# Kernel tuning notes

Hardware: AMD Instinct MI355X
Metric: run time of the kernel (lower is better)

The kernel has to match this reference:

```python
import jax, jax.numpy as jnp
import numpy as np
import math

HIDDEN = 1024
HEADS = 16
HEAD_DIM = HIDDEN // HEADS
B, S = 2, 2048


def _xavier(key, shape):
    fan_in, fan_out = shape[1], shape[0]
    limit = math.sqrt(6.0 / (fan_in + fan_out))
    return jax.random.uniform(key, shape, jnp.float32, -limit, limit)


def setup_inputs() -> dict:
    key = jax.random.key(0)
    ks = jax.random.split(key, 5)
    x = jax.random.normal(ks[0], (B, S, HIDDEN), jnp.float32)
    # torch Linear stores weight as [out, in]; y = x @ W.T + b
    Wq = _xavier(ks[1], (HIDDEN, HIDDEN))
    Wk = _xavier(ks[2], (HIDDEN, HIDDEN))
    Wv = _xavier(ks[3], (HIDDEN, HIDDEN))
    Wo = _xavier(ks[4], (HIDDEN, HIDDEN))
    bq = jnp.zeros((HIDDEN,), jnp.float32)
    bk = jnp.zeros((HIDDEN,), jnp.float32)
    bv = jnp.zeros((HIDDEN,), jnp.float32)
    bo = jnp.zeros((HIDDEN,), jnp.float32)
    return {"x": x, "Wq": Wq, "bq": bq, "Wk": Wk, "bk": bk,
            "Wv": Wv, "bv": bv, "Wo": Wo, "bo": bo}


def reference(x, Wq, bq, Wk, bk, Wv, bv, Wo, bo):
    b, s, d = x.shape
    h, hd = HEADS, HEAD_DIM
    q = (x @ Wq.T + bq).reshape(b, s, h, hd).transpose(0, 2, 1, 3)  # [b,h,s,hd]
    k = (x @ Wk.T + bk).reshape(b, s, h, hd).transpose(0, 2, 1, 3)
    v = (x @ Wv.T + bv).reshape(b, s, h, hd).transpose(0, 2, 1, 3)
    scores = jnp.einsum('bhqd,bhkd->bhqk', q, k) / math.sqrt(hd)
    causal = jnp.tril(jnp.ones((s, s), bool))
    scores = jnp.where(causal, scores, -jnp.inf)
    attn = jax.nn.softmax(scores, axis=-1)
    out = jnp.einsum('bhqk,bhkd->bhqd', attn, v)  # [b,h,s,hd]
    out = out.transpose(0, 2, 1, 3).reshape(b, s, d)
    return out @ Wo.T + bo
```

## Files before the change

### kernel.cpp

```cpp
#include <hip/hip_runtime.h>
#include <hip/hip_bf16.h>


typedef __hip_bfloat16 bf16;
typedef __attribute__((ext_vector_type(8))) short short8;
typedef __attribute__((ext_vector_type(4))) short short4v;
typedef __attribute__((ext_vector_type(4))) float f32x4;

#define MFMA16(a, b, c) __builtin_amdgcn_mfma_f32_16x16x32_bf16((a), (b), (c), 0, 0, 0)

__device__ __forceinline__ void load_lds16(const void* g, void* l) {
  __builtin_amdgcn_global_load_lds(
      (const __attribute__((address_space(1))) void*)g,
      (__attribute__((address_space(3))) void*)l, 16, 0, 0);
}

__global__ __launch_bounds__(256) void cvt_kernel(
    const float* __restrict__ x, const float* __restrict__ wq,
    const float* __restrict__ wk, const float* __restrict__ wv,
    const float* __restrict__ wo, bf16* __restrict__ xb, bf16* __restrict__ wqb,
    bf16* __restrict__ wkb, bf16* __restrict__ wvb, bf16* __restrict__ wob) {
  const int seg = blockIdx.y;
  const float* src;
  bf16* dst;
  int n;
  if (seg == 0)      { src = x;  dst = xb;  n = 4194304; }
  else if (seg == 1) { src = wq; dst = wqb; n = 1048576; }
  else if (seg == 2) { src = wk; dst = wkb; n = 1048576; }
  else if (seg == 3) { src = wv; dst = wvb; n = 1048576; }
  else               { src = wo; dst = wob; n = 1048576; }
  const int i = (blockIdx.x * 256 + threadIdx.x) * 4;
  if (i >= n) return;
  const float4 v = *(const float4*)(src + i);
  short4v p;
  ((bf16*)&p)[0] = __float2bfloat16(v.x);
  ((bf16*)&p)[1] = __float2bfloat16(v.y);
  ((bf16*)&p)[2] = __float2bfloat16(v.z);
  ((bf16*)&p)[3] = __float2bfloat16(v.w);
  *(short4v*)(dst + i) = p;
}

template <int BM, typename OutT, bool TRANS>
__device__ __forceinline__ void gemm_body(const bf16* __restrict__ X,
                                          const bf16* __restrict__ W,
                                          const float* __restrict__ bias,
                                          OutT* __restrict__ Y, float scale) {
  constexpr int K = 1024, N = 1024;
  constexpr int MI = BM / 32;
  __shared__ bf16 As[BM * 32];
  __shared__ bf16 Bs[128 * 32];
  const int t = threadIdx.x;
  const int lane = t & 63, w = t >> 6;
  const int quad = lane >> 4, r = lane & 15;
  const int m0 = blockIdx.y * BM, n0 = blockIdx.x * 128;
  const int wm = w >> 1, wn = w & 1;

  f32x4 acc[MI][4] = {};

  for (int k0 = 0; k0 < K; k0 += 32) {
    __syncthreads();
#pragma unroll
    for (int p = 0; p < BM / 64; ++p) {
      const int c = p * 256 + w * 64 + lane;
      const int row = c >> 2;
      const int scb = (c & 3) ^ ((row >> 1) & 3);
      load_lds16(X + (size_t)(m0 + row) * K + k0 + scb * 8, As + c * 8);
    }
#pragma unroll
    for (int p = 0; p < 2; ++p) {
      const int c = p * 256 + w * 64 + lane;
      const int row = c >> 2;
      const int scb = (c & 3) ^ ((row >> 1) & 3);
      load_lds16(W + (size_t)(n0 + row) * K + k0 + scb * 8, Bs + c * 8);
    }
    __syncthreads();
    short8 af[MI], bfr[4];
#pragma unroll
    for (int i = 0; i < MI; ++i) {
      const int ra = wm * (MI * 16) + i * 16 + r;
      af[i] = *(const short8*)(As + ra * 32 + ((quad ^ ((ra >> 1) & 3)) * 8));
    }
#pragma unroll
    for (int j = 0; j < 4; ++j) {
      const int rb = wn * 64 + j * 16 + r;
      bfr[j] = *(const short8*)(Bs + rb * 32 + ((quad ^ ((rb >> 1) & 3)) * 8));
    }
#pragma unroll
    for (int i = 0; i < MI; ++i)
#pragma unroll
      for (int j = 0; j < 4; ++j)
        acc[i][j] = MFMA16(af[i], bfr[j], acc[i][j]);
  }
#pragma unroll
  for (int i = 0; i < MI; ++i) {
    const int m = m0 + wm * (MI * 16) + i * 16 + quad * 4;
#pragma unroll
    for (int j = 0; j < 4; ++j) {
      const int n = n0 + wn * 64 + j * 16 + r;
      const float bv = bias[n];
      if constexpr (TRANS) {
        short4v pk;
#pragma unroll
        for (int g = 0; g < 4; ++g)
          ((bf16*)&pk)[g] = __float2bfloat16((acc[i][j][g] + bv) * scale);
        *(short4v*)((bf16*)Y + (size_t)n * 4096 + m) = pk;
      } else {
#pragma unroll
        for (int g = 0; g < 4; ++g) {
          const float val = (acc[i][j][g] + bv) * scale;
          if constexpr (__is_same(OutT, float))
            Y[(size_t)(m + g) * N + n] = val;
          else
            Y[(size_t)(m + g) * N + n] = __float2bfloat16(val);
        }
      }
    }
  }
}

#define QSCALE 0.18033688f

__global__ __launch_bounds__(256) void qkv_kernel(
    const bf16* __restrict__ x, const bf16* __restrict__ Wq,
    const float* __restrict__ bq, const bf16* __restrict__ Wk,
    const float* __restrict__ bk, const bf16* __restrict__ Wv,
    const float* __restrict__ bv, bf16* Qb, bf16* Kb, bf16* Vtg) {
  if (blockIdx.z == 0)      gemm_body<128, bf16, false>(x, Wq, bq, Qb, QSCALE);
  else if (blockIdx.z == 1) gemm_body<128, bf16, false>(x, Wk, bk, Kb, 1.0f);
  else                      gemm_body<128, bf16, true >(x, Wv, bv, Vtg, 1.0f);
}

__global__ __launch_bounds__(256) void proj_kernel(const bf16* __restrict__ X,
                                                   const bf16* __restrict__ W,
                                                   const float* __restrict__ bias,
                                                   float* __restrict__ Y) {
  gemm_body<64, float, false>(X, W, bias, Y, 1.0f);
}

__global__ __launch_bounds__(256) void attn_kernel(const bf16* __restrict__ Qb,
                                                   const bf16* __restrict__ Kb,
                                                   const bf16* __restrict__ Vtg,
                                                   bf16* __restrict__ Ob) {
  const int pair = blockIdx.x, h = blockIdx.y, b = blockIdx.z;
  const int t = threadIdx.x;
  const int lane = t & 63, w = t >> 6;
  const int quad = lane >> 4, r = lane & 15;

  __shared__ bf16 Ks[64 * 64];
  __shared__ bf16 Vt[64 * 64];
  __shared__ bf16 Pl[4][16 * 64];

#pragma unroll 1
  for (int sel = 0; sel < 2; ++sel) {
    const int j = sel ? (31 - pair) : pair;
    const int q0 = j * 64;
    const int qrow = q0 + w * 16 + r;

    short8 qf[2];
#pragma unroll
    for (int ks = 0; ks < 2; ++ks)
      qf[ks] = *(const short8*)(Qb + (size_t)(b * 2048 + qrow) * 1024 + h * 64 +
                                ks * 32 + quad * 8);

    f32x4 o[4] = {};
    float mrow = -1e30f, lrow = 0.f;

    for (int kt = 0; kt <= j; ++kt) {
      const int k0 = kt * 64;
      __syncthreads();
#pragma unroll
      for (int p = 0; p < 2; ++p) {
        const int c = p * 256 + w * 64 + lane;
        const int row = c >> 3;
        const int scb = (c & 7) ^ (row & 7);
        load_lds16(Kb + (size_t)(b * 2048 + k0 + row) * 1024 + h * 64 + scb * 8,
                   Ks + c * 8);
      }
#pragma unroll
      for (int p = 0; p < 2; ++p) {
        const int c = p * 256 + w * 64 + lane;
        const int row = c >> 3;
        const int scb = (c & 7) ^ (row & 7);
        load_lds16(Vtg + (size_t)(h * 64 + row) * 4096 + b * 2048 + k0 + scb * 8,
                   Vt + c * 8);
      }
      __syncthreads();

      f32x4 st[4] = {};
#pragma unroll
      for (int ks = 0; ks < 2; ++ks) {
        short8 kf[4];
#pragma unroll
        for (int mt = 0; mt < 4; ++mt) {
          const int key = mt * 16 + r;
          kf[mt] = *(const short8*)(Ks + key * 64 +
                                    (((ks * 4 + quad) ^ (key & 7)) * 8));
        }
#pragma unroll
        for (int mt = 0; mt < 4; ++mt) st[mt] = MFMA16(kf[mt], qf[ks], st[mt]);
      }

      if (kt == j) {
#pragma unroll
        for (int mt = 0; mt < 4; ++mt)
#pragma unroll
          for (int g = 0; g < 4; ++g) {
            const int key = k0 + mt * 16 + quad * 4 + g;
            if (key > qrow) st[mt][g] = -1e30f;
          }
      }

      float mx = -1e30f;
#pragma unroll
      for (int mt = 0; mt < 4; ++mt)
#pragma unroll
        for (int g = 0; g < 4; ++g) mx = fmaxf(mx, st[mt][g]);
      mx = fmaxf(mx, __shfl_xor(mx, 16));
      mx = fmaxf(mx, __shfl_xor(mx, 32));
      const float mnew = fmaxf(mrow, mx);
      const float alpha = exp2f(mrow - mnew);
      mrow = mnew;
      float sum = 0.f;
#pragma unroll
      for (int mt = 0; mt < 4; ++mt) {
        bf16 pk[4];
#pragma unroll
        for (int g = 0; g < 4; ++g) {
          const float p = exp2f(st[mt][g] - mnew);
          pk[g] = __float2bfloat16(p);
          sum += __bfloat162float(pk[g]);
        }
        const int key8 = mt * 2 + (quad >> 1);
        const int off = r * 64 + ((key8 ^ (r & 7)) * 8) + (quad & 1) * 4;
        *(short4v*)(&Pl[w][off]) = *(const short4v*)pk;
      }
      sum += __shfl_xor(sum, 16);
      sum += __shfl_xor(sum, 32);
      lrow = lrow * alpha + sum;
#pragma unroll
      for (int mt = 0; mt < 4; ++mt)
#pragma unroll
        for (int g = 0; g < 4; ++g) o[mt][g] *= alpha;

      asm volatile("s_waitcnt lgkmcnt(0)" ::: "memory");

#pragma unroll
      for (int ks = 0; ks < 2; ++ks) {
        short8 vf[4], pf;
#pragma unroll
        for (int mt = 0; mt < 4; ++mt) {
          const int d = mt * 16 + r;
          vf[mt] = *(const short8*)(Vt + d * 64 +
                                    (((ks * 4 + quad) ^ (d & 7)) * 8));
        }
        pf = *(const short8*)(Pl[w] + r * 64 + (((ks * 4 + quad) ^ (r & 7)) * 8));
#pragma unroll
        for (int mt = 0; mt < 4; ++mt) o[mt] = MFMA16(vf[mt], pf, o[mt]);
      }
    }

    const float inv = 1.f / lrow;
#pragma unroll
    for (int mt = 0; mt < 4; ++mt) {
      const int d0 = mt * 16 + quad * 4;
      short4v pk;
#pragma unroll
      for (int g = 0; g < 4; ++g)
        ((bf16*)&pk)[g] = __float2bfloat16(o[mt][g] * inv);
      *(short4v*)(Ob + (size_t)(b * 2048 + qrow) * 1024 + h * 64 + d0) = pk;
    }
  }
}

extern "C" void kernel_launch(void* const* d_in, const int* in_sizes, int n_in,
                              void* d_out, int out_size, void* d_ws, size_t ws_size,
                              hipStream_t stream) {
  const float* x  = (const float*)d_in[0];
  const float* Wq = (const float*)d_in[1];
  const float* bq = (const float*)d_in[2];
  const float* Wk = (const float*)d_in[3];
  const float* bk = (const float*)d_in[4];
  const float* Wv = (const float*)d_in[5];
  const float* bv = (const float*)d_in[6];
  const float* Wo = (const float*)d_in[7];
  const float* bo = (const float*)d_in[8];
  float* out = (float*)d_out;

  bf16* xb  = (bf16*)d_ws;
  bf16* wqb = xb  + (size_t)4096 * 1024;
  bf16* wkb = wqb + (size_t)1024 * 1024;
  bf16* wvb = wkb + (size_t)1024 * 1024;
  bf16* wob = wvb + (size_t)1024 * 1024;
  bf16* Qb  = wob + (size_t)1024 * 1024;
  bf16* Kb  = Qb  + (size_t)4096 * 1024;
  bf16* Vtg = Kb  + (size_t)4096 * 1024;
  bf16* Ob  = Vtg + (size_t)4096 * 1024;
  const size_t need = ((size_t)4096 * 1024 * 5 + (size_t)1024 * 1024 * 4) * 2;
  if (ws_size < need) return;

  cvt_kernel<<<dim3(4096, 5), 256, 0, stream>>>(x, Wq, Wk, Wv, Wo,
                                                xb, wqb, wkb, wvb, wob);
  qkv_kernel<<<dim3(8, 32, 3), 256, 0, stream>>>(xb, wqb, bq, wkb, bk, wvb, bv,
                                                 Qb, Kb, Vtg);
  attn_kernel<<<dim3(16, 16, 2), 256, 0, stream>>>(Qb, Kb, Vtg, Ob);
  proj_kernel<<<dim3(8, 64, 1), 256, 0, stream>>>(Ob, wob, bo, out);
}
```

Baseline: 203.7 us.

## Double-buffer LDS tiles in GEMM and attention loops to prefetch next tile

Both the projection GEMM and the flash-attention kernel now keep two LDS buffers for their staged tiles. The next K-slice (GEMM) or next K/V tile (attention) is issued with global_load_lds right after the barrier, so the loads overlap the MFMA work on the current buffer. This also removes one barrier per iteration. The cost is double the LDS footprint, which may lower occupancy. Correctness relies on the barrier waiting for the outstanding async LDS loads before the buffer is consumed.

```diff
diff --git a/kernel.cpp b/kernel.cpp
--- a/kernel.cpp
+++ b/kernel.cpp
@@ -47,8 +47,8 @@
                                           OutT* __restrict__ Y, float scale) {
   constexpr int K = 1024, N = 1024;
   constexpr int MI = BM / 32;
-  __shared__ bf16 As[BM * 32];
-  __shared__ bf16 Bs[128 * 32];
+  __shared__ bf16 As[2][BM * 32];
+  __shared__ bf16 Bs[2][128 * 32];
   const int t = threadIdx.x;
   const int lane = t & 63, w = t >> 6;
   const int quad = lane >> 4, r = lane & 15;
@@ -57,33 +57,38 @@
 
   f32x4 acc[MI][4] = {};
 
-  for (int k0 = 0; k0 < K; k0 += 32) {
-    __syncthreads();
+  auto stage = [&](int k0, int buf) {
 #pragma unroll
     for (int p = 0; p < BM / 64; ++p) {
       const int c = p * 256 + w * 64 + lane;
       const int row = c >> 2;
       const int scb = (c & 3) ^ ((row >> 1) & 3);
-      load_lds16(X + (size_t)(m0 + row) * K + k0 + scb * 8, As + c * 8);
+      load_lds16(X + (size_t)(m0 + row) * K + k0 + scb * 8, As[buf] + c * 8);
     }
 #pragma unroll
     for (int p = 0; p < 2; ++p) {
       const int c = p * 256 + w * 64 + lane;
       const int row = c >> 2;
       const int scb = (c & 3) ^ ((row >> 1) & 3);
-      load_lds16(W + (size_t)(n0 + row) * K + k0 + scb * 8, Bs + c * 8);
-    }
+      load_lds16(W + (size_t)(n0 + row) * K + k0 + scb * 8, Bs[buf] + c * 8);
+    }
+  };
+
+  stage(0, 0);
+  int cur = 0;
+  for (int k0 = 0; k0 < K; k0 += 32, cur ^= 1) {
     __syncthreads();
+    if (k0 + 32 < K) stage(k0 + 32, cur ^ 1);
     short8 af[MI], bfr[4];
 #pragma unroll
     for (int i = 0; i < MI; ++i) {
       const int ra = wm * (MI * 16) + i * 16 + r;
-      af[i] = *(const short8*)(As + ra * 32 + ((quad ^ ((ra >> 1) & 3)) * 8));
+      af[i] = *(const short8*)(As[cur] + ra * 32 + ((quad ^ ((ra >> 1) & 3)) * 8));
     }
 #pragma unroll
     for (int j = 0; j < 4; ++j) {
       const int rb = wn * 64 + j * 16 + r;
-      bfr[j] = *(const short8*)(Bs + rb * 32 + ((quad ^ ((rb >> 1) & 3)) * 8));
+      bfr[j] = *(const short8*)(Bs[cur] + rb * 32 + ((quad ^ ((rb >> 1) & 3)) * 8));
     }
 #pragma unroll
     for (int i = 0; i < MI; ++i)
@@ -146,9 +151,28 @@
   const int lane = t & 63, w = t >> 6;
   const int quad = lane >> 4, r = lane & 15;
 
-  __shared__ bf16 Ks[64 * 64];
-  __shared__ bf16 Vt[64 * 64];
+  __shared__ bf16 Ks[2][64 * 64];
+  __shared__ bf16 Vt[2][64 * 64];
   __shared__ bf16 Pl[4][16 * 64];
+
+  auto stageKV = [&](int k0, int buf) {
+#pragma unroll
+    for (int p = 0; p < 2; ++p) {
+      const int c = p * 256 + w * 64 + lane;
+      const int row = c >> 3;
+      const int scb = (c & 7) ^ (row & 7);
+      load_lds16(Kb + (size_t)(b * 2048 + k0 + row) * 1024 + h * 64 + scb * 8,
+                 Ks[buf] + c * 8);
+    }
+#pragma unroll
+    for (int p = 0; p < 2; ++p) {
+      const int c = p * 256 + w * 64 + lane;
+      const int row = c >> 3;
+      const int scb = (c & 7) ^ (row & 7);
+      load_lds16(Vtg + (size_t)(h * 64 + row) * 4096 + b * 2048 + k0 + scb * 8,
+                 Vt[buf] + c * 8);
+    }
+  };
 
 #pragma unroll 1
   for (int sel = 0; sel < 2; ++sel) {
@@ -165,26 +189,14 @@
     f32x4 o[4] = {};
     float mrow = -1e30f, lrow = 0.f;
 
-    for (int kt = 0; kt <= j; ++kt) {
+    __syncthreads();
+    stageKV(0, 0);
+    int cur = 0;
+
+    for (int kt = 0; kt <= j; ++kt, cur ^= 1) {
       const int k0 = kt * 64;
       __syncthreads();
-#pragma unroll
-      for (int p = 0; p < 2; ++p) {
-        const int c = p * 256 + w * 64 + lane;
-        const int row = c >> 3;
-        const int scb = (c & 7) ^ (row & 7);
-        load_lds16(Kb + (size_t)(b * 2048 + k0 + row) * 1024 + h * 64 + scb * 8,
-                   Ks + c * 8);
-      }
-#pragma unroll
-      for (int p = 0; p < 2; ++p) {
-        const int c = p * 256 + w * 64 + lane;
-        const int row = c >> 3;
-        const int scb = (c & 7) ^ (row & 7);
-        load_lds16(Vtg + (size_t)(h * 64 + row) * 4096 + b * 2048 + k0 + scb * 8,
-                   Vt + c * 8);
-      }
-      __syncthreads();
+      if (kt < j) stageKV(k0 + 64, cur ^ 1);
 
       f32x4 st[4] = {};
 #pragma unroll
@@ -193,7 +205,7 @@
 #pragma unroll
         for (int mt = 0; mt < 4; ++mt) {
           const int key = mt * 16 + r;
-          kf[mt] = *(const short8*)(Ks + key * 64 +
+          kf[mt] = *(const short8*)(Ks[cur] + key * 64 +
                                     (((ks * 4 + quad) ^ (key & 7)) * 8));
         }
 #pragma unroll
@@ -250,7 +262,7 @@
 #pragma unroll
         for (int mt = 0; mt < 4; ++mt) {
           const int d = mt * 16 + r;
-          vf[mt] = *(const short8*)(Vt + d * 64 +
+          vf[mt] = *(const short8*)(Vt[cur] + d * 64 +
                                     (((ks * 4 + quad) ^ (d & 7)) * 8));
         }
         pf = *(const short8*)(Pl[w] + r * 64 + (((ks * 4 + quad) ^ (r & 7)) * 8));
```

New measurement: 221.7 us. 8.9% more time.
